# Kernel optimization log

Measured on AMD Instinct MI355X. Metric: run time of the kernel, lower is better.

Reference implementation:

```python
import jax, jax.numpy as jnp
import numpy as np

NUM_EXPERTS = 64
TOP_K = 6
EP_SIZE = 8
EP_RANK = 0
N_LOCAL = NUM_EXPERTS // EP_SIZE  # 8 local experts on this rank
HIDDEN = 2048
INTER = 1408
BLOCK_N = 128
BLOCK_K = 128
T = 2048  # tokens


def setup_inputs() -> dict:
    key = jax.random.key(0)
    ks = jax.random.split(key, 6)
    return {
        "x": jax.random.normal(ks[0], (T, HIDDEN), jnp.float32),
        "router_logits": jax.random.normal(ks[1], (T, NUM_EXPERTS), jnp.float32),
        "w13": jax.random.normal(ks[2], (N_LOCAL, 2 * INTER, HIDDEN), jnp.float32) * 0.02,
        "w13_scale": jax.random.uniform(ks[3], (N_LOCAL, 2 * INTER // BLOCK_N, HIDDEN // BLOCK_K), jnp.float32, 0.5, 1.5),
        "w2": jax.random.normal(ks[4], (N_LOCAL, HIDDEN, INTER), jnp.float32) * 0.02,
        "w2_scale": jax.random.uniform(ks[5], (N_LOCAL, HIDDEN // BLOCK_N, INTER // BLOCK_K), jnp.float32, 0.5, 1.5),
    }


def _dequant(w, s, bn, bk):
    # block-quantized weight dequant: w[e, n, k] * s[e, n//bn, k//bk]
    s_full = jnp.repeat(jnp.repeat(s, bn, axis=1), bk, axis=2)
    return w * s_full


def reference(x, router_logits, w13, w13_scale, w2, w2_scale):
    # --- top-k routing (softmax -> topk -> renormalize) ---
    probs = jax.nn.softmax(router_logits, axis=-1)           # [T, E]
    topk_w, topk_ids = jax.lax.top_k(probs, TOP_K)           # [T, K]
    topk_w = topk_w / jnp.sum(topk_w, axis=-1, keepdims=True)
    # --- expert-id remap to local partition (balanced map: e % ep_size) ---
    eids = jnp.arange(NUM_EXPERTS)
    expert_id_to_local = jnp.where(eids % EP_SIZE == EP_RANK, eids // EP_SIZE, -1)
    local_ids = expert_id_to_local[topk_ids]                 # [T, K], -1 if off-rank
    valid = local_ids >= 0
    # combine weights per local expert: comb[t, e] = sum_k topk_w[t,k] * [local==e]
    tok = jnp.arange(x.shape[0])[:, None]
    comb = jnp.zeros((x.shape[0], N_LOCAL), x.dtype).at[
        tok, jnp.where(valid, local_ids, 0)
    ].add(jnp.where(valid, topk_w, 0.0))
    # --- dequantize block-quantized weights ---
    w13_dq = _dequant(w13, w13_scale, BLOCK_N, BLOCK_K)      # [E, 2I, H]
    w2_dq = _dequant(w2, w2_scale, BLOCK_N, BLOCK_K)         # [E, H, I]
    # --- grouped GEMM (dense over local experts, masked by comb) ---
    h = jnp.einsum('th,enh->etn', x, w13_dq)                 # [E, T, 2I]
    gate, up = h[..., :INTER], h[..., INTER:]
    a = jax.nn.silu(gate) * up                               # [E, T, I]
    o = jnp.einsum('etn,ehn->eth', a, w2_dq)                 # [E, T, H]
    return jnp.einsum('eth,te->th', o, comb)                 # [T, H]
```

## Files before the change

### kernel.cpp

```cpp
#include <hip/hip_runtime.h>
#include <hip/hip_bf16.h>
#include <cstdint>

#define T_TOK 2048
#define HID   2048
#define NEXP  64
#define TOPK  6
#define NLOC  8
#define ITR   1408
#define ITR2  2816
#define NSLOT (T_TOK * TOPK)
#define NK1   32
#define NK2   22

#define OFF_CNT   0
#define OFF_CNT2  32
#define OFF_OFFS  64
#define OFF_TOPID 4096
#define OFF_TOPW  (OFF_TOPID + T_TOK * TOPK * 4)
#define OFF_TOK   (OFF_TOPW  + T_TOK * TOPK * 4)
#define OFF_WOF   (OFF_TOK   + NSLOT * 4)
#define OFF_XBF   (OFF_WOF   + NSLOT * 4)
#define OFF_ABUF  (OFF_XBF   + (size_t)T_TOK * HID * 2)

typedef __attribute__((ext_vector_type(4))) float f32x4;
typedef __attribute__((ext_vector_type(8))) short s16x8;
typedef __attribute__((ext_vector_type(4))) short s16x4;

__device__ __forceinline__ short f2bf(float f) {
    union { float f; unsigned u; } v; v.f = f;
    unsigned r = v.u + 0x7FFFu + ((v.u >> 16) & 1u);
    return (short)(r >> 16);
}

__global__ __launch_bounds__(256) void k_zero(float* __restrict__ out,
                                              int* __restrict__ cnt)
{
    const int idx = blockIdx.x * 256 + threadIdx.x;
    float4 z = {0.f, 0.f, 0.f, 0.f};
    #pragma unroll
    for (int p = 0; p < 4; ++p)
        *(float4*)&out[(size_t)(idx + p * 262144) * 4] = z;
    if (blockIdx.x == 0 && threadIdx.x < 16) cnt[threadIdx.x] = 0;
}

__global__ __launch_bounds__(256) void k_route(
    const float* __restrict__ logits, int* __restrict__ cnt,
    int* __restrict__ top_ids, float* __restrict__ top_w)
{
    const int lane = threadIdx.x & 63;
    const int t = blockIdx.x * 4 + (threadIdx.x >> 6);

    float v = logits[t * NEXP + lane];
    float m = v;
    #pragma unroll
    for (int s = 32; s > 0; s >>= 1) m = fmaxf(m, __shfl_xor(m, s));
    float ev = expf(v - m);
    float ssum = ev;
    #pragma unroll
    for (int s = 32; s > 0; s >>= 1) ssum += __shfl_xor(ssum, s);
    float p = ev / ssum;

    float pv = p;
    int ids[TOPK]; float wsel[TOPK]; float wsum = 0.f;
    #pragma unroll
    for (int i = 0; i < TOPK; ++i) {
        float mx = pv;
        #pragma unroll
        for (int s = 32; s > 0; s >>= 1) mx = fmaxf(mx, __shfl_xor(mx, s));
        unsigned long long b = __ballot(pv == mx);
        int idx = (int)__builtin_ctzll(b);
        float w = __shfl(p, idx);
        ids[i] = idx; wsel[i] = w; wsum += w;
        if (lane == idx) pv = -1.0f;
    }
    if (lane < TOPK) {
        top_ids[t * TOPK + lane] = ids[lane];
        top_w[t * TOPK + lane]  = wsel[lane] / wsum;
    }
    if (lane == 0) {
        #pragma unroll
        for (int i = 0; i < TOPK; ++i)
            if ((ids[i] & 7) == 0) atomicAdd(&cnt[ids[i] >> 3], 1);
    }
}

__global__ void k_offsets(int* __restrict__ cnt, int* __restrict__ cnt2,
                          int* __restrict__ offs)
{
    if (threadIdx.x == 0) {
        int s = 0;
        for (int e = 0; e < NLOC; ++e) { offs[e] = s; s += cnt[e]; cnt2[e] = 0; }
    }
}

__global__ __launch_bounds__(256) void k_scatter(
    const int* __restrict__ top_ids, const float* __restrict__ top_w,
    const int* __restrict__ offs, int* __restrict__ cnt2,
    int* __restrict__ tok_of, float* __restrict__ w_of)
{
    const int t = blockIdx.x * 256 + threadIdx.x;
    #pragma unroll
    for (int i = 0; i < TOPK; ++i) {
        int id = top_ids[t * TOPK + i];
        if ((id & 7) == 0) {
            int e = id >> 3;
            int s = offs[e] + atomicAdd(&cnt2[e], 1);
            tok_of[s] = t;
            w_of[s]  = top_w[t * TOPK + i];
        }
    }
}

__global__ __launch_bounds__(256) void k_cvt_x(const float* __restrict__ x,
                                               short* __restrict__ xbf)
{
    const int r = blockIdx.x;
    const int c = threadIdx.x * 8;
    const float4 a = *(const float4*)&x[(size_t)r * HID + c];
    const float4 b = *(const float4*)&x[(size_t)r * HID + c + 4];
    s16x8 v = { f2bf(a.x), f2bf(a.y), f2bf(a.z), f2bf(a.w),
                f2bf(b.x), f2bf(b.y), f2bf(b.z), f2bf(b.w) };
    *(s16x8*)&xbf[(size_t)r * HID + c] = v;
}

__global__ __launch_bounds__(256, 2) void k_gemm1(
    const short* __restrict__ xbf, const float* __restrict__ w13,
    const float* __restrict__ w13s, const int* __restrict__ offs,
    const int* __restrict__ cnt, const int* __restrict__ tok_of,
    short* __restrict__ a_buf)
{
    const int b = blockIdx.x;
    const int e = b & 7;
    const int tt = b >> 3;
    const int cntE = cnt[e];
    const int m0 = (tt / 44) * 256;
    if (m0 >= cntE) return;
    const int n0p = (tt % 44) * 32;
    const int base = offs[e] + m0;
    const int tid = threadIdx.x;
    const int lane = tid & 63;
    const int wm = tid >> 6;

    __shared__ __align__(16) short As[2][256 * 64];
    __shared__ __align__(16) short Ws[2][64 * 64];

    int* tokp = (int*)&As[0][0];
    tokp[tid] = tok_of[base + ((m0 + tid < cntE) ? tid : 0)];
    __syncthreads();

    const short* aptr[8];
    int aoff[8];
    #pragma unroll
    for (int p = 0; p < 8; ++p) {
        const int row = p * 32 + (tid >> 3), cg = tid & 7;
        aptr[p] = xbf + (size_t)tokp[row] * HID + cg * 8;
        aoff[p] = (row * 64 + cg * 8) ^ ((row & 7) << 3);
    }
    __syncthreads();

    const float* wptr[4];
    int woff[4];
    {
        const float* wg = w13 + ((size_t)e * ITR2 + n0p) * HID;
        const float* wu = w13 + ((size_t)e * ITR2 + ITR + n0p) * HID;
        #pragma unroll
        for (int p = 0; p < 4; ++p) {
            const int row = p * 16 + (tid >> 4), ch = tid & 15;
            wptr[p] = ((p < 2) ? wg : wu) + (size_t)(row & 31) * HID + ch * 4;
            woff[p] = (row * 64 + ch * 4) ^ ((row & 7) << 3);
        }
    }
    const int sgi = (e * 22 + (n0p >> 7)) * 16;
    const int sui = (e * 22 + 11 + (n0p >> 7)) * 16;

    s16x8 ra[8];
    float4 rw[4];
    float sgv, suv;
    f32x4 acc[2][2][4] = {};

#define G1_LOAD(kk) do {                                                       \
    const int k0 = (kk) * 64;                                                  \
    sgv = w13s[sgi + ((kk) >> 1)];                                             \
    suv = w13s[sui + ((kk) >> 1)];                                             \
    _Pragma("unroll")                                                          \
    for (int p = 0; p < 8; ++p) ra[p] = *(const s16x8*)(aptr[p] + k0);         \
    _Pragma("unroll")                                                          \
    for (int p = 0; p < 4; ++p) rw[p] = *(const float4*)(wptr[p] + k0);        \
} while (0)

#define G1_WRITE(b) do {                                                       \
    _Pragma("unroll")                                                          \
    for (int p = 0; p < 8; ++p) *(s16x8*)&As[b][aoff[p]] = ra[p];              \
    _Pragma("unroll")                                                          \
    for (int p = 0; p < 4; ++p) {                                              \
        const float s = (p < 2) ? sgv : suv;                                   \
        s16x4 v = { f2bf(rw[p].x * s), f2bf(rw[p].y * s),                      \
                    f2bf(rw[p].z * s), f2bf(rw[p].w * s) };                    \
        *(s16x4*)&Ws[b][woff[p]] = v;                                          \
    }                                                                          \
} while (0)

#define G1_COMP(b) do {                                                        \
    _Pragma("unroll")                                                          \
    for (int ks = 0; ks < 2; ++ks) {                                           \
        const int co = ks * 32 + (lane >> 4) * 8;                              \
        s16x8 af[4];                                                           \
        _Pragma("unroll")                                                      \
        for (int mf = 0; mf < 4; ++mf) {                                       \
            const int row = wm * 64 + mf * 16 + (lane & 15);                   \
            af[mf] = *(const s16x8*)&As[b][(row * 64 + co) ^ ((row & 7) << 3)];\
        }                                                                      \
        _Pragma("unroll")                                                      \
        for (int t = 0; t < 2; ++t)                                            \
        _Pragma("unroll")                                                      \
        for (int nf = 0; nf < 2; ++nf) {                                       \
            const int row = t * 32 + nf * 16 + (lane & 15);                    \
            s16x8 bv = *(const s16x8*)&Ws[b][(row * 64 + co) ^ ((row & 7) << 3)];\
            _Pragma("unroll")                                                  \
            for (int mf = 0; mf < 4; ++mf)                                     \
                acc[t][nf][mf] = __builtin_amdgcn_mfma_f32_16x16x32_bf16(af[mf], bv, acc[t][nf][mf], 0, 0, 0); \
        }                                                                      \
    }                                                                          \
} while (0)

    G1_LOAD(0);
    G1_WRITE(0);
    __syncthreads();
    #pragma unroll 2
    for (int k = 0; k < NK1; ++k) {
        if (k + 1 < NK1) G1_LOAD(k + 1);
        G1_COMP(k & 1);
        if (k + 1 < NK1) {
            G1_WRITE((k & 1) ^ 1);
            __syncthreads();
        }
    }

    #pragma unroll
    for (int nf = 0; nf < 2; ++nf) {
        const int col = n0p + nf * 16 + (lane & 15);
        #pragma unroll
        for (int mf = 0; mf < 4; ++mf)
        #pragma unroll
        for (int j = 0; j < 4; ++j) {
            const int row = wm * 64 + mf * 16 + (lane >> 4) * 4 + j;
            if (m0 + row < cntE) {
                const float g = acc[0][nf][mf][j], u = acc[1][nf][mf][j];
                const float a = (g / (1.f + __expf(-g))) * u;
                a_buf[(size_t)(base + row) * ITR + col] = f2bf(a);
            }
        }
    }
#undef G1_LOAD
#undef G1_WRITE
#undef G1_COMP
}

__global__ __launch_bounds__(256, 2) void k_gemm2(
    const short* __restrict__ a_buf, const float* __restrict__ w2,
    const float* __restrict__ w2s, const int* __restrict__ offs,
    const int* __restrict__ cnt, const int* __restrict__ tok_of,
    const float* __restrict__ w_of, float* __restrict__ out)
{
    const int b = blockIdx.x;
    const int e = b & 7;
    const int tt = b >> 3;
    const int cntE = cnt[e];
    const int m0 = (tt / 64) * 256;
    if (m0 >= cntE) return;
    const int n0 = (tt % 64) * 32;
    const int base = offs[e] + m0;
    const int tid = threadIdx.x;
    const int lane = tid & 63;
    const int wm = tid >> 6;

    __shared__ __align__(16) short As[2][256 * 64];
    __shared__ __align__(16) short Ws[2][32 * 64];

    const short* aptr[8];
    int aoff[8];
    #pragma unroll
    for (int p = 0; p < 8; ++p) {
        const int row = p * 32 + (tid >> 3), cg = tid & 7;
        int srow = base + row; if (srow > NSLOT - 1) srow = NSLOT - 1;
        aptr[p] = a_buf + (size_t)srow * ITR + cg * 8;
        aoff[p] = (row * 64 + cg * 8) ^ ((row & 7) << 3);
    }
    const float* wptr[2];
    int woff[2];
    #pragma unroll
    for (int p = 0; p < 2; ++p) {
        const int row = p * 16 + (tid >> 4), ch = tid & 15;
        wptr[p] = w2 + ((size_t)e * HID + n0 + row) * ITR + ch * 4;
        woff[p] = (row * 64 + ch * 4) ^ ((row & 7) << 3);
    }
    const int sci = (e * 16 + (n0 >> 7)) * 11;

    s16x8 ra[8];
    float4 rw[2];
    float scv;
    f32x4 acc[2][4] = {};

#define G2_LOAD(kk) do {                                                       \
    const int k0 = (kk) * 64;                                                  \
    scv = w2s[sci + ((kk) >> 1)];                                              \
    _Pragma("unroll")                                                          \
    for (int p = 0; p < 8; ++p) ra[p] = *(const s16x8*)(aptr[p] + k0);         \
    _Pragma("unroll")                                                          \
    for (int p = 0; p < 2; ++p) rw[p] = *(const float4*)(wptr[p] + k0);        \
} while (0)

#define G2_WRITE(b) do {                                                       \
    _Pragma("unroll")                                                          \
    for (int p = 0; p < 8; ++p) *(s16x8*)&As[b][aoff[p]] = ra[p];              \
    _Pragma("unroll")                                                          \
    for (int p = 0; p < 2; ++p) {                                              \
        s16x4 v = { f2bf(rw[p].x * scv), f2bf(rw[p].y * scv),                  \
                    f2bf(rw[p].z * scv), f2bf(rw[p].w * scv) };                \
        *(s16x4*)&Ws[b][woff[p]] = v;                                          \
    }                                                                          \
} while (0)

#define G2_COMP(b) do {                                                        \
    _Pragma("unroll")                                                          \
    for (int ks = 0; ks < 2; ++ks) {                                           \
        const int co = ks * 32 + (lane >> 4) * 8;                              \
        s16x8 af[4];                                                           \
        _Pragma("unroll")                                                      \
        for (int mf = 0; mf < 4; ++mf) {                                       \
            const int row = wm * 64 + mf * 16 + (lane & 15);                   \
            af[mf] = *(const s16x8*)&As[b][(row * 64 + co) ^ ((row & 7) << 3)];\
        }                                                                      \
        _Pragma("unroll")                                                      \
        for (int nf = 0; nf < 2; ++nf) {                                       \
            const int row = nf * 16 + (lane & 15);                             \
            s16x8 bv = *(const s16x8*)&Ws[b][(row * 64 + co) ^ ((row & 7) << 3)];\
            _Pragma("unroll")                                                  \
            for (int mf = 0; mf < 4; ++mf)                                     \
                acc[nf][mf] = __builtin_amdgcn_mfma_f32_16x16x32_bf16(af[mf], bv, acc[nf][mf], 0, 0, 0); \
        }                                                                      \
    }                                                                          \
} while (0)

    G2_LOAD(0);
    G2_WRITE(0);
    __syncthreads();
    #pragma unroll 2
    for (int k = 0; k < NK2; ++k) {
        if (k + 1 < NK2) G2_LOAD(k + 1);
        G2_COMP(k & 1);
        if (k + 1 < NK2) {
            G2_WRITE((k & 1) ^ 1);
            __syncthreads();
        }
    }

    #pragma unroll
    for (int mf = 0; mf < 4; ++mf)
    #pragma unroll
    for (int j = 0; j < 4; ++j) {
        const int row = wm * 64 + mf * 16 + (lane >> 4) * 4 + j;
        if (m0 + row < cntE) {
            const int   t = tok_of[base + row];
            const float w = w_of[base + row];
            #pragma unroll
            for (int nf = 0; nf < 2; ++nf) {
                const int col = n0 + nf * 16 + (lane & 15);
                atomicAdd(&out[(size_t)t * HID + col], acc[nf][mf][j] * w);
            }
        }
    }
#undef G2_LOAD
#undef G2_WRITE
#undef G2_COMP
}

extern "C" void kernel_launch(void* const* d_in, const int* in_sizes, int n_in,
                              void* d_out, int out_size, void* d_ws, size_t ws_size,
                              hipStream_t stream)
{
    const float* x      = (const float*)d_in[0];
    const float* logits = (const float*)d_in[1];
    const float* w13    = (const float*)d_in[2];
    const float* w13s   = (const float*)d_in[3];
    const float* w2     = (const float*)d_in[4];
    const float* w2s    = (const float*)d_in[5];
    float* out = (float*)d_out;
    char*  ws  = (char*)d_ws;

    int*   cnt     = (int*)(ws + OFF_CNT);
    int*   cnt2    = (int*)(ws + OFF_CNT2);
    int*   offs    = (int*)(ws + OFF_OFFS);
    int*   top_ids = (int*)(ws + OFF_TOPID);
    float* top_w   = (float*)(ws + OFF_TOPW);
    int*   tok_of  = (int*)(ws + OFF_TOK);
    float* w_of    = (float*)(ws + OFF_WOF);
    short* xbf     = (short*)(ws + OFF_XBF);
    short* a_buf   = (short*)(ws + OFF_ABUF);

    k_zero   <<<1024,        256, 0, stream>>>(out, cnt);
    k_route  <<<T_TOK / 4,   256, 0, stream>>>(logits, cnt, top_ids, top_w);
    k_offsets<<<1,            64, 0, stream>>>(cnt, cnt2, offs);
    k_scatter<<<T_TOK / 256, 256, 0, stream>>>(top_ids, top_w, offs, cnt2, tok_of, w_of);
    k_cvt_x  <<<T_TOK,       256, 0, stream>>>(x, xbf);
    k_gemm1  <<<44 * 8 * NLOC, 256, 0, stream>>>(xbf, w13, w13s, offs, cnt, tok_of, a_buf);
    k_gemm2  <<<64 * 8 * NLOC, 256, 0, stream>>>(a_buf, w2, w2s, offs, cnt, tok_of, w_of, out);
}
```

Baseline: 168.3 us.

## Fuse prep kernels, inline expert offsets, and pipeline GEMM loads across LDS-only barriers

Folds x-to-bf16 conversion and output zeroing into one prep kernel. Drops the single-thread offsets kernel: each scatter and GEMM block now recomputes its expert offset from the counts, which removes two kernel launches. Both GEMMs get explicit two-set register double buffering and a custom barrier that waits only on LDS counters. Outstanding global loads for the next tile can then stay in flight across the barrier, where __syncthreads would wait for them. This raises register pressure under the 2-blocks-per-CU launch bound and depends on the compiler inserting correct vmcnt waits before the register values are used.

After: 192.3 us. 1.14x slower.

```diff
diff --git a/kernel.cpp b/kernel.cpp
--- a/kernel.cpp
+++ b/kernel.cpp
@@ -33,15 +33,28 @@
     return (short)(r >> 16);
 }
 
-__global__ __launch_bounds__(256) void k_zero(float* __restrict__ out,
+#define BAR() do {                                            \
+    asm volatile("s_waitcnt lgkmcnt(0)" ::: "memory");        \
+    __builtin_amdgcn_s_barrier();                             \
+    asm volatile("" ::: "memory");                            \
+} while (0)
+
+__global__ __launch_bounds__(256) void k_prep(const float* __restrict__ x,
+                                              short* __restrict__ xbf,
+                                              float* __restrict__ out,
                                               int* __restrict__ cnt)
 {
-    const int idx = blockIdx.x * 256 + threadIdx.x;
+    const int r = blockIdx.x;
+    const int c = threadIdx.x * 8;
+    const float4 a = *(const float4*)&x[(size_t)r * HID + c];
+    const float4 b = *(const float4*)&x[(size_t)r * HID + c + 4];
+    s16x8 v = { f2bf(a.x), f2bf(a.y), f2bf(a.z), f2bf(a.w),
+                f2bf(b.x), f2bf(b.y), f2bf(b.z), f2bf(b.w) };
+    *(s16x8*)&xbf[(size_t)r * HID + c] = v;
     float4 z = {0.f, 0.f, 0.f, 0.f};
-    #pragma unroll
-    for (int p = 0; p < 4; ++p)
-        *(float4*)&out[(size_t)(idx + p * 262144) * 4] = z;
-    if (blockIdx.x == 0 && threadIdx.x < 16) cnt[threadIdx.x] = 0;
+    *(float4*)&out[(size_t)r * HID + c] = z;
+    *(float4*)&out[(size_t)r * HID + c + 4] = z;
+    if (r == 0 && threadIdx.x < 16) cnt[threadIdx.x] = 0;
 }
 
 __global__ __launch_bounds__(256) void k_route(
@@ -85,21 +98,18 @@
     }
 }
 
-__global__ void k_offsets(int* __restrict__ cnt, int* __restrict__ cnt2,
-                          int* __restrict__ offs)
-{
-    if (threadIdx.x == 0) {
-        int s = 0;
-        for (int e = 0; e < NLOC; ++e) { offs[e] = s; s += cnt[e]; cnt2[e] = 0; }
-    }
-}
-
 __global__ __launch_bounds__(256) void k_scatter(
     const int* __restrict__ top_ids, const float* __restrict__ top_w,
-    const int* __restrict__ offs, int* __restrict__ cnt2,
+    const int* __restrict__ cnt, int* __restrict__ cnt2,
     int* __restrict__ tok_of, float* __restrict__ w_of)
 {
     const int t = blockIdx.x * 256 + threadIdx.x;
+    int offs[NLOC];
+    {
+        int s = 0;
+        #pragma unroll
+        for (int i = 0; i < NLOC; ++i) { offs[i] = s; s += cnt[i]; }
+    }
     #pragma unroll
     for (int i = 0; i < TOPK; ++i) {
         int id = top_ids[t * TOPK + i];
@@ -112,32 +122,21 @@
     }
 }
 
-__global__ __launch_bounds__(256) void k_cvt_x(const float* __restrict__ x,
-                                               short* __restrict__ xbf)
-{
-    const int r = blockIdx.x;
-    const int c = threadIdx.x * 8;
-    const float4 a = *(const float4*)&x[(size_t)r * HID + c];
-    const float4 b = *(const float4*)&x[(size_t)r * HID + c + 4];
-    s16x8 v = { f2bf(a.x), f2bf(a.y), f2bf(a.z), f2bf(a.w),
-                f2bf(b.x), f2bf(b.y), f2bf(b.z), f2bf(b.w) };
-    *(s16x8*)&xbf[(size_t)r * HID + c] = v;
-}
-
 __global__ __launch_bounds__(256, 2) void k_gemm1(
     const short* __restrict__ xbf, const float* __restrict__ w13,
-    const float* __restrict__ w13s, const int* __restrict__ offs,
-    const int* __restrict__ cnt, const int* __restrict__ tok_of,
-    short* __restrict__ a_buf)
+    const float* __restrict__ w13s, const int* __restrict__ cnt,
+    const int* __restrict__ tok_of, short* __restrict__ a_buf)
 {
     const int b = blockIdx.x;
     const int e = b & 7;
     const int tt = b >> 3;
-    const int cntE = cnt[e];
+    int off_e = 0, cntE = 0;
+    #pragma unroll
+    for (int i = 0; i < NLOC; ++i) { int c = cnt[i]; if (i < e) off_e += c; if (i == e) cntE = c; }
     const int m0 = (tt / 44) * 256;
     if (m0 >= cntE) return;
     const int n0p = (tt % 44) * 32;
-    const int base = offs[e] + m0;
+    const int base = off_e + m0;
     const int tid = threadIdx.x;
     const int lane = tid & 63;
     const int wm = tid >> 6;
@@ -147,7 +146,7 @@
 
     int* tokp = (int*)&As[0][0];
     tokp[tid] = tok_of[base + ((m0 + tid < cntE) ? tid : 0)];
-    __syncthreads();
+    BAR();
 
     const short* aptr[8];
     int aoff[8];
@@ -157,7 +156,7 @@
         aptr[p] = xbf + (size_t)tokp[row] * HID + cg * 8;
         aoff[p] = (row * 64 + cg * 8) ^ ((row & 7) << 3);
     }
-    __syncthreads();
+    BAR();
 
     const float* wptr[4];
     int woff[4];
@@ -174,29 +173,29 @@
     const int sgi = (e * 22 + (n0p >> 7)) * 16;
     const int sui = (e * 22 + 11 + (n0p >> 7)) * 16;
 
-    s16x8 ra[8];
-    float4 rw[4];
-    float sgv, suv;
+    s16x8 ra0[8], ra1[8];
+    float4 rw0[4], rw1[4];
+    float sg0, su0, sg1, su1;
     f32x4 acc[2][2][4] = {};
 
-#define G1_LOAD(kk) do {                                                       \
+#define G1_LOAD(kk, S) do {                                                    \
     const int k0 = (kk) * 64;                                                  \
-    sgv = w13s[sgi + ((kk) >> 1)];                                             \
-    suv = w13s[sui + ((kk) >> 1)];                                             \
-    _Pragma("unroll")                                                          \
-    for (int p = 0; p < 8; ++p) ra[p] = *(const s16x8*)(aptr[p] + k0);         \
-    _Pragma("unroll")                                                          \
-    for (int p = 0; p < 4; ++p) rw[p] = *(const float4*)(wptr[p] + k0);        \
-} while (0)
-
-#define G1_WRITE(b) do {                                                       \
-    _Pragma("unroll")                                                          \
-    for (int p = 0; p < 8; ++p) *(s16x8*)&As[b][aoff[p]] = ra[p];              \
+    sg##S = w13s[sgi + ((kk) >> 1)];                                           \
+    su##S = w13s[sui + ((kk) >> 1)];                                           \
+    _Pragma("unroll")                                                          \
+    for (int p = 0; p < 8; ++p) ra##S[p] = *(const s16x8*)(aptr[p] + k0);      \
+    _Pragma("unroll")                                                          \
+    for (int p = 0; p < 4; ++p) rw##S[p] = *(const float4*)(wptr[p] + k0);     \
+} while (0)
+
+#define G1_WRITE(b, S) do {                                                    \
+    _Pragma("unroll")                                                          \
+    for (int p = 0; p < 8; ++p) *(s16x8*)&As[b][aoff[p]] = ra##S[p];           \
     _Pragma("unroll")                                                          \
     for (int p = 0; p < 4; ++p) {                                              \
-        const float s = (p < 2) ? sgv : suv;                                   \
-        s16x4 v = { f2bf(rw[p].x * s), f2bf(rw[p].y * s),                      \
-                    f2bf(rw[p].z * s), f2bf(rw[p].w * s) };                    \
+        const float s = (p < 2) ? sg##S : su##S;                               \
+        s16x4 v = { f2bf(rw##S[p].x * s), f2bf(rw##S[p].y * s),                \
+                    f2bf(rw##S[p].z * s), f2bf(rw##S[p].w * s) };              \
         *(s16x4*)&Ws[b][woff[p]] = v;                                          \
     }                                                                          \
 } while (0)
@@ -224,18 +223,24 @@
     }                                                                          \
 } while (0)
 
-    G1_LOAD(0);
-    G1_WRITE(0);
-    __syncthreads();
-    #pragma unroll 2
-    for (int k = 0; k < NK1; ++k) {
-        if (k + 1 < NK1) G1_LOAD(k + 1);
-        G1_COMP(k & 1);
-        if (k + 1 < NK1) {
-            G1_WRITE((k & 1) ^ 1);
-            __syncthreads();
-        }
-    }
+    G1_LOAD(0, 0);
+    G1_WRITE(0, 0);
+    G1_LOAD(1, 1);
+    BAR();
+    for (int k = 0; k < NK1 - 2; k += 2) {
+        G1_LOAD(k + 2, 0);
+        G1_COMP(0);
+        G1_WRITE(1, 1);
+        BAR();
+        G1_LOAD(k + 3, 1);
+        G1_COMP(1);
+        G1_WRITE(0, 0);
+        BAR();
+    }
+    G1_COMP(0);
+    G1_WRITE(1, 1);
+    BAR();
+    G1_COMP(1);
 
     #pragma unroll
     for (int nf = 0; nf < 2; ++nf) {
@@ -259,18 +264,20 @@
 
 __global__ __launch_bounds__(256, 2) void k_gemm2(
     const short* __restrict__ a_buf, const float* __restrict__ w2,
-    const float* __restrict__ w2s, const int* __restrict__ offs,
-    const int* __restrict__ cnt, const int* __restrict__ tok_of,
-    const float* __restrict__ w_of, float* __restrict__ out)
+    const float* __restrict__ w2s, const int* __restrict__ cnt,
+    const int* __restrict__ tok_of, const float* __restrict__ w_of,
+    float* __restrict__ out)
 {
     const int b = blockIdx.x;
     const int e = b & 7;
     const int tt = b >> 3;
-    const int cntE = cnt[e];
+    int off_e = 0, cntE = 0;
+    #pragma unroll
+    for (int i = 0; i < NLOC; ++i) { int c = cnt[i]; if (i < e) off_e += c; if (i == e) cntE = c; }
     const int m0 = (tt / 64) * 256;
     if (m0 >= cntE) return;
     const int n0 = (tt % 64) * 32;
-    const int base = offs[e] + m0;
+    const int base = off_e + m0;
     const int tid = threadIdx.x;
     const int lane = tid & 63;
     const int wm = tid >> 6;
@@ -297,27 +304,27 @@
     }
     const int sci = (e * 16 + (n0 >> 7)) * 11;
 
-    s16x8 ra[8];
-    float4 rw[2];
-    float scv;
+    s16x8 ra0[8], ra1[8];
+    float4 rw0[2], rw1[2];
+    float sc0, sc1;
     f32x4 acc[2][4] = {};
 
-#define G2_LOAD(kk) do {                                                       \
+#define G2_LOAD(kk, S) do {                                                    \
     const int k0 = (kk) * 64;                                                  \
-    scv = w2s[sci + ((kk) >> 1)];                                              \
-    _Pragma("unroll")                                                          \
-    for (int p = 0; p < 8; ++p) ra[p] = *(const s16x8*)(aptr[p] + k0);         \
-    _Pragma("unroll")                                                          \
-    for (int p = 0; p < 2; ++p) rw[p] = *(const float4*)(wptr[p] + k0);        \
-} while (0)
-
-#define G2_WRITE(b) do {                                                       \
-    _Pragma("unroll")                                                          \
-    for (int p = 0; p < 8; ++p) *(s16x8*)&As[b][aoff[p]] = ra[p];              \
+    sc##S = w2s[sci + ((kk) >> 1)];                                            \
+    _Pragma("unroll")                                                          \
+    for (int p = 0; p < 8; ++p) ra##S[p] = *(const s16x8*)(aptr[p] + k0);      \
+    _Pragma("unroll")                                                          \
+    for (int p = 0; p < 2; ++p) rw##S[p] = *(const float4*)(wptr[p] + k0);     \
+} while (0)
+
+#define G2_WRITE(b, S) do {                                                    \
+    _Pragma("unroll")                                                          \
+    for (int p = 0; p < 8; ++p) *(s16x8*)&As[b][aoff[p]] = ra##S[p];           \
     _Pragma("unroll")                                                          \
     for (int p = 0; p < 2; ++p) {                                              \
-        s16x4 v = { f2bf(rw[p].x * scv), f2bf(rw[p].y * scv),                  \
-                    f2bf(rw[p].z * scv), f2bf(rw[p].w * scv) };                \
+        s16x4 v = { f2bf(rw##S[p].x * sc##S), f2bf(rw##S[p].y * sc##S),        \
+                    f2bf(rw##S[p].z * sc##S), f2bf(rw##S[p].w * sc##S) };      \
         *(s16x4*)&Ws[b][woff[p]] = v;                                          \
     }                                                                          \
 } while (0)
@@ -343,18 +350,24 @@
     }                                                                          \
 } while (0)
 
-    G2_LOAD(0);
-    G2_WRITE(0);
-    __syncthreads();
-    #pragma unroll 2
-    for (int k = 0; k < NK2; ++k) {
-        if (k + 1 < NK2) G2_LOAD(k + 1);
-        G2_COMP(k & 1);
-        if (k + 1 < NK2) {
-            G2_WRITE((k & 1) ^ 1);
-            __syncthreads();
-        }
-    }
+    G2_LOAD(0, 0);
+    G2_WRITE(0, 0);
+    G2_LOAD(1, 1);
+    BAR();
+    for (int k = 0; k < NK2 - 2; k += 2) {
+        G2_LOAD(k + 2, 0);
+        G2_COMP(0);
+        G2_WRITE(1, 1);
+        BAR();
+        G2_LOAD(k + 3, 1);
+        G2_COMP(1);
+        G2_WRITE(0, 0);
+        BAR();
+    }
+    G2_COMP(0);
+    G2_WRITE(1, 1);
+    BAR();
+    G2_COMP(1);
 
     #pragma unroll
     for (int mf = 0; mf < 4; ++mf)
@@ -391,7 +404,6 @@
 
     int*   cnt     = (int*)(ws + OFF_CNT);
     int*   cnt2    = (int*)(ws + OFF_CNT2);
-    int*   offs    = (int*)(ws + OFF_OFFS);
     int*   top_ids = (int*)(ws + OFF_TOPID);
     float* top_w   = (float*)(ws + OFF_TOPW);
     int*   tok_of  = (int*)(ws + OFF_TOK);
@@ -399,11 +411,9 @@
     short* xbf     = (short*)(ws + OFF_XBF);
     short* a_buf   = (short*)(ws + OFF_ABUF);
 
-    k_zero   <<<1024,        256, 0, stream>>>(out, cnt);
+    k_prep   <<<T_TOK,       256, 0, stream>>>(x, xbf, out, cnt);
     k_route  <<<T_TOK / 4,   256, 0, stream>>>(logits, cnt, top_ids, top_w);
-    k_offsets<<<1,            64, 0, stream>>>(cnt, cnt2, offs);
-    k_scatter<<<T_TOK / 256, 256, 0, stream>>>(top_ids, top_w, offs, cnt2, tok_of, w_of);
-    k_cvt_x  <<<T_TOK,       256, 0, stream>>>(x, xbf);
-    k_gemm1  <<<44 * 8 * NLOC, 256, 0, stream>>>(xbf, w13, w13s, offs, cnt, tok_of, a_buf);
-    k_gemm2  <<<64 * 8 * NLOC, 256, 0, stream>>>(a_buf, w2, w2s, offs, cnt, tok_of, w_of, out);
-}
+    k_scatter<<<T_TOK / 256, 256, 0, stream>>>(top_ids, top_w, cnt, cnt2, tok_of, w_of);
+    k_gemm1  <<<44 * 8 * NLOC, 256, 0, stream>>>(xbf, w13, w13s, cnt, tok_of, a_buf);
+    k_gemm2  <<<64 * 8 * NLOC, 256, 0, stream>>>(a_buf, w2, w2s, cnt, tok_of, w_of, out);
+}
```

## Halve GEMM M-tile, fuse zero/convert kernels, inline expert offsets

Applied to the files above, without the earlier changes.

Both grouped-GEMM kernels drop from 256-row to 128-row token tiles. This doubles the block grid and raises the occupancy hint (3 and 4 blocks per CU) to improve parallelism and reduce padding waste for roughly 190 tokens per expert. The output-zeroing and x-to-bf16 conversion kernels are merged into one, and the separate offsets kernel is removed: each consumer now computes its expert's prefix sum from the counts. The cost is that each weight tile may be streamed twice per expert, which adds fp32 weight traffic unless the second read hits in cache.

New measurement: 141.6 us. -15.9%, faster.

```diff
diff --git a/kernel.cpp b/kernel.cpp
--- a/kernel.cpp
+++ b/kernel.cpp
@@ -15,7 +15,6 @@
 
 #define OFF_CNT   0
 #define OFF_CNT2  32
-#define OFF_OFFS  64
 #define OFF_TOPID 4096
 #define OFF_TOPW  (OFF_TOPID + T_TOK * TOPK * 4)
 #define OFF_TOK   (OFF_TOPW  + T_TOK * TOPK * 4)
@@ -33,15 +32,22 @@
     return (short)(r >> 16);
 }
 
-__global__ __launch_bounds__(256) void k_zero(float* __restrict__ out,
+__global__ __launch_bounds__(256) void k_prep(const float* __restrict__ x,
+                                              short* __restrict__ xbf,
+                                              float* __restrict__ out,
                                               int* __restrict__ cnt)
 {
-    const int idx = blockIdx.x * 256 + threadIdx.x;
+    const int r = blockIdx.x;
+    const int c = threadIdx.x * 8;
+    const float4 a = *(const float4*)&x[(size_t)r * HID + c];
+    const float4 b = *(const float4*)&x[(size_t)r * HID + c + 4];
+    s16x8 v = { f2bf(a.x), f2bf(a.y), f2bf(a.z), f2bf(a.w),
+                f2bf(b.x), f2bf(b.y), f2bf(b.z), f2bf(b.w) };
+    *(s16x8*)&xbf[(size_t)r * HID + c] = v;
     float4 z = {0.f, 0.f, 0.f, 0.f};
-    #pragma unroll
-    for (int p = 0; p < 4; ++p)
-        *(float4*)&out[(size_t)(idx + p * 262144) * 4] = z;
-    if (blockIdx.x == 0 && threadIdx.x < 16) cnt[threadIdx.x] = 0;
+    *(float4*)&out[(size_t)r * HID + c] = z;
+    *(float4*)&out[(size_t)r * HID + c + 4] = z;
+    if (r == 0 && threadIdx.x < 16) cnt[threadIdx.x] = 0;
 }
 
 __global__ __launch_bounds__(256) void k_route(
@@ -85,21 +91,18 @@
     }
 }
 
-__global__ void k_offsets(int* __restrict__ cnt, int* __restrict__ cnt2,
-                          int* __restrict__ offs)
-{
-    if (threadIdx.x == 0) {
-        int s = 0;
-        for (int e = 0; e < NLOC; ++e) { offs[e] = s; s += cnt[e]; cnt2[e] = 0; }
-    }
-}
-
 __global__ __launch_bounds__(256) void k_scatter(
     const int* __restrict__ top_ids, const float* __restrict__ top_w,
-    const int* __restrict__ offs, int* __restrict__ cnt2,
+    const int* __restrict__ cnt, int* __restrict__ cnt2,
     int* __restrict__ tok_of, float* __restrict__ w_of)
 {
     const int t = blockIdx.x * 256 + threadIdx.x;
+    int offs[NLOC];
+    {
+        int s = 0;
+        #pragma unroll
+        for (int i = 0; i < NLOC; ++i) { offs[i] = s; s += cnt[i]; }
+    }
     #pragma unroll
     for (int i = 0; i < TOPK; ++i) {
         int id = top_ids[t * TOPK + i];
@@ -112,47 +115,36 @@
     }
 }
 
-__global__ __launch_bounds__(256) void k_cvt_x(const float* __restrict__ x,
-                                               short* __restrict__ xbf)
-{
-    const int r = blockIdx.x;
-    const int c = threadIdx.x * 8;
-    const float4 a = *(const float4*)&x[(size_t)r * HID + c];
-    const float4 b = *(const float4*)&x[(size_t)r * HID + c + 4];
-    s16x8 v = { f2bf(a.x), f2bf(a.y), f2bf(a.z), f2bf(a.w),
-                f2bf(b.x), f2bf(b.y), f2bf(b.z), f2bf(b.w) };
-    *(s16x8*)&xbf[(size_t)r * HID + c] = v;
-}
-
-__global__ __launch_bounds__(256, 2) void k_gemm1(
+__global__ __launch_bounds__(256, 3) void k_gemm1(
     const short* __restrict__ xbf, const float* __restrict__ w13,
-    const float* __restrict__ w13s, const int* __restrict__ offs,
-    const int* __restrict__ cnt, const int* __restrict__ tok_of,
-    short* __restrict__ a_buf)
+    const float* __restrict__ w13s, const int* __restrict__ cnt,
+    const int* __restrict__ tok_of, short* __restrict__ a_buf)
 {
     const int b = blockIdx.x;
     const int e = b & 7;
     const int tt = b >> 3;
-    const int cntE = cnt[e];
-    const int m0 = (tt / 44) * 256;
+    int off_e = 0, cntE = 0;
+    #pragma unroll
+    for (int i = 0; i < NLOC; ++i) { int c = cnt[i]; if (i < e) off_e += c; if (i == e) cntE = c; }
+    const int m0 = (tt / 44) * 128;
     if (m0 >= cntE) return;
     const int n0p = (tt % 44) * 32;
-    const int base = offs[e] + m0;
+    const int base = off_e + m0;
     const int tid = threadIdx.x;
     const int lane = tid & 63;
     const int wm = tid >> 6;
 
-    __shared__ __align__(16) short As[2][256 * 64];
+    __shared__ __align__(16) short As[2][128 * 64];
     __shared__ __align__(16) short Ws[2][64 * 64];
 
     int* tokp = (int*)&As[0][0];
-    tokp[tid] = tok_of[base + ((m0 + tid < cntE) ? tid : 0)];
+    if (tid < 128) tokp[tid] = tok_of[base + ((m0 + tid < cntE) ? tid : 0)];
     __syncthreads();
 
-    const short* aptr[8];
-    int aoff[8];
-    #pragma unroll
-    for (int p = 0; p < 8; ++p) {
+    const short* aptr[4];
+    int aoff[4];
+    #pragma unroll
+    for (int p = 0; p < 4; ++p) {
         const int row = p * 32 + (tid >> 3), cg = tid & 7;
         aptr[p] = xbf + (size_t)tokp[row] * HID + cg * 8;
         aoff[p] = (row * 64 + cg * 8) ^ ((row & 7) << 3);
@@ -174,24 +166,24 @@
     const int sgi = (e * 22 + (n0p >> 7)) * 16;
     const int sui = (e * 22 + 11 + (n0p >> 7)) * 16;
 
-    s16x8 ra[8];
+    s16x8 ra[4];
     float4 rw[4];
     float sgv, suv;
-    f32x4 acc[2][2][4] = {};
+    f32x4 acc[2][2][2] = {};
 
 #define G1_LOAD(kk) do {                                                       \
     const int k0 = (kk) * 64;                                                  \
     sgv = w13s[sgi + ((kk) >> 1)];                                             \
     suv = w13s[sui + ((kk) >> 1)];                                             \
     _Pragma("unroll")                                                          \
-    for (int p = 0; p < 8; ++p) ra[p] = *(const s16x8*)(aptr[p] + k0);         \
+    for (int p = 0; p < 4; ++p) ra[p] = *(const s16x8*)(aptr[p] + k0);         \
     _Pragma("unroll")                                                          \
     for (int p = 0; p < 4; ++p) rw[p] = *(const float4*)(wptr[p] + k0);        \
 } while (0)
 
 #define G1_WRITE(b) do {                                                       \
     _Pragma("unroll")                                                          \
-    for (int p = 0; p < 8; ++p) *(s16x8*)&As[b][aoff[p]] = ra[p];              \
+    for (int p = 0; p < 4; ++p) *(s16x8*)&As[b][aoff[p]] = ra[p];              \
     _Pragma("unroll")                                                          \
     for (int p = 0; p < 4; ++p) {                                              \
         const float s = (p < 2) ? sgv : suv;                                   \
@@ -205,10 +197,10 @@
     _Pragma("unroll")                                                          \
     for (int ks = 0; ks < 2; ++ks) {                                           \
         const int co = ks * 32 + (lane >> 4) * 8;                              \
-        s16x8 af[4];                                                           \
+        s16x8 af[2];                                                           \
         _Pragma("unroll")                                                      \
-        for (int mf = 0; mf < 4; ++mf) {                                       \
-            const int row = wm * 64 + mf * 16 + (lane & 15);                   \
+        for (int mf = 0; mf < 2; ++mf) {                                       \
+            const int row = wm * 32 + mf * 16 + (lane & 15);                   \
             af[mf] = *(const s16x8*)&As[b][(row * 64 + co) ^ ((row & 7) << 3)];\
         }                                                                      \
         _Pragma("unroll")                                                      \
@@ -218,7 +210,7 @@
             const int row = t * 32 + nf * 16 + (lane & 15);                    \
             s16x8 bv = *(const s16x8*)&Ws[b][(row * 64 + co) ^ ((row & 7) << 3)];\
             _Pragma("unroll")                                                  \
-            for (int mf = 0; mf < 4; ++mf)                                     \
+            for (int mf = 0; mf < 2; ++mf)                                     \
                 acc[t][nf][mf] = __builtin_amdgcn_mfma_f32_16x16x32_bf16(af[mf], bv, acc[t][nf][mf], 0, 0, 0); \
         }                                                                      \
     }                                                                          \
@@ -241,10 +233,10 @@
     for (int nf = 0; nf < 2; ++nf) {
         const int col = n0p + nf * 16 + (lane & 15);
         #pragma unroll
-        for (int mf = 0; mf < 4; ++mf)
+        for (int mf = 0; mf < 2; ++mf)
         #pragma unroll
         for (int j = 0; j < 4; ++j) {
-            const int row = wm * 64 + mf * 16 + (lane >> 4) * 4 + j;
+            const int row = wm * 32 + mf * 16 + (lane >> 4) * 4 + j;
             if (m0 + row < cntE) {
                 const float g = acc[0][nf][mf][j], u = acc[1][nf][mf][j];
                 const float a = (g / (1.f + __expf(-g))) * u;
@@ -257,31 +249,33 @@
 #undef G1_COMP
 }
 
-__global__ __launch_bounds__(256, 2) void k_gemm2(
+__global__ __launch_bounds__(256, 4) void k_gemm2(
     const short* __restrict__ a_buf, const float* __restrict__ w2,
-    const float* __restrict__ w2s, const int* __restrict__ offs,
-    const int* __restrict__ cnt, const int* __restrict__ tok_of,
-    const float* __restrict__ w_of, float* __restrict__ out)
+    const float* __restrict__ w2s, const int* __restrict__ cnt,
+    const int* __restrict__ tok_of, const float* __restrict__ w_of,
+    float* __restrict__ out)
 {
     const int b = blockIdx.x;
     const int e = b & 7;
     const int tt = b >> 3;
-    const int cntE = cnt[e];
-    const int m0 = (tt / 64) * 256;
+    int off_e = 0, cntE = 0;
+    #pragma unroll
+    for (int i = 0; i < NLOC; ++i) { int c = cnt[i]; if (i < e) off_e += c; if (i == e) cntE = c; }
+    const int m0 = (tt / 64) * 128;
     if (m0 >= cntE) return;
     const int n0 = (tt % 64) * 32;
-    const int base = offs[e] + m0;
+    const int base = off_e + m0;
     const int tid = threadIdx.x;
     const int lane = tid & 63;
     const int wm = tid >> 6;
 
-    __shared__ __align__(16) short As[2][256 * 64];
+    __shared__ __align__(16) short As[2][128 * 64];
     __shared__ __align__(16) short Ws[2][32 * 64];
 
-    const short* aptr[8];
-    int aoff[8];
-    #pragma unroll
-    for (int p = 0; p < 8; ++p) {
+    const short* aptr[4];
+    int aoff[4];
+    #pragma unroll
+    for (int p = 0; p < 4; ++p) {
         const int row = p * 32 + (tid >> 3), cg = tid & 7;
         int srow = base + row; if (srow > NSLOT - 1) srow = NSLOT - 1;
         aptr[p] = a_buf + (size_t)srow * ITR + cg * 8;
@@ -297,23 +291,23 @@
     }
     const int sci = (e * 16 + (n0 >> 7)) * 11;
 
-    s16x8 ra[8];
+    s16x8 ra[4];
     float4 rw[2];
     float scv;
-    f32x4 acc[2][4] = {};
+    f32x4 acc[2][2] = {};
 
 #define G2_LOAD(kk) do {                                                       \
     const int k0 = (kk) * 64;                                                  \
     scv = w2s[sci + ((kk) >> 1)];                                              \
     _Pragma("unroll")                                                          \
-    for (int p = 0; p < 8; ++p) ra[p] = *(const s16x8*)(aptr[p] + k0);         \
+    for (int p = 0; p < 4; ++p) ra[p] = *(const s16x8*)(aptr[p] + k0);         \
     _Pragma("unroll")                                                          \
     for (int p = 0; p < 2; ++p) rw[p] = *(const float4*)(wptr[p] + k0);        \
 } while (0)
 
 #define G2_WRITE(b) do {                                                       \
     _Pragma("unroll")                                                          \
-    for (int p = 0; p < 8; ++p) *(s16x8*)&As[b][aoff[p]] = ra[p];              \
+    for (int p = 0; p < 4; ++p) *(s16x8*)&As[b][aoff[p]] = ra[p];              \
     _Pragma("unroll")                                                          \
     for (int p = 0; p < 2; ++p) {                                              \
         s16x4 v = { f2bf(rw[p].x * scv), f2bf(rw[p].y * scv),                  \
@@ -326,10 +320,10 @@
     _Pragma("unroll")                                                          \
     for (int ks = 0; ks < 2; ++ks) {                                           \
         const int co = ks * 32 + (lane >> 4) * 8;                              \
-        s16x8 af[4];                                                           \
+        s16x8 af[2];                                                           \
         _Pragma("unroll")                                                      \
-        for (int mf = 0; mf < 4; ++mf) {                                       \
-            const int row = wm * 64 + mf * 16 + (lane & 15);                   \
+        for (int mf = 0; mf < 2; ++mf) {                                       \
+            const int row = wm * 32 + mf * 16 + (lane & 15);                   \
             af[mf] = *(const s16x8*)&As[b][(row * 64 + co) ^ ((row & 7) << 3)];\
         }                                                                      \
         _Pragma("unroll")                                                      \
@@ -337,7 +331,7 @@
             const int row = nf * 16 + (lane & 15);                             \
             s16x8 bv = *(const s16x8*)&Ws[b][(row * 64 + co) ^ ((row & 7) << 3)];\
             _Pragma("unroll")                                                  \
-            for (int mf = 0; mf < 4; ++mf)                                     \
+            for (int mf = 0; mf < 2; ++mf)                                     \
                 acc[nf][mf] = __builtin_amdgcn_mfma_f32_16x16x32_bf16(af[mf], bv, acc[nf][mf], 0, 0, 0); \
         }                                                                      \
     }                                                                          \
@@ -357,10 +351,10 @@
     }
 
     #pragma unroll
-    for (int mf = 0; mf < 4; ++mf)
+    for (int mf = 0; mf < 2; ++mf)
     #pragma unroll
     for (int j = 0; j < 4; ++j) {
-        const int row = wm * 64 + mf * 16 + (lane >> 4) * 4 + j;
+        const int row = wm * 32 + mf * 16 + (lane >> 4) * 4 + j;
         if (m0 + row < cntE) {
             const int   t = tok_of[base + row];
             const float w = w_of[base + row];
@@ -391,7 +385,6 @@
 
     int*   cnt     = (int*)(ws + OFF_CNT);
     int*   cnt2    = (int*)(ws + OFF_CNT2);
-    int*   offs    = (int*)(ws + OFF_OFFS);
     int*   top_ids = (int*)(ws + OFF_TOPID);
     float* top_w   = (float*)(ws + OFF_TOPW);
     int*   tok_of  = (int*)(ws + OFF_TOK);
@@ -399,11 +392,9 @@
     short* xbf     = (short*)(ws + OFF_XBF);
     short* a_buf   = (short*)(ws + OFF_ABUF);
 
-    k_zero   <<<1024,        256, 0, stream>>>(out, cnt);
+    k_prep   <<<T_TOK,       256, 0, stream>>>(x, xbf, out, cnt);
     k_route  <<<T_TOK / 4,   256, 0, stream>>>(logits, cnt, top_ids, top_w);
-    k_offsets<<<1,            64, 0, stream>>>(cnt, cnt2, offs);
-    k_scatter<<<T_TOK / 256, 256, 0, stream>>>(top_ids, top_w, offs, cnt2, tok_of, w_of);
-    k_cvt_x  <<<T_TOK,       256, 0, stream>>>(x, xbf);
-    k_gemm1  <<<44 * 8 * NLOC, 256, 0, stream>>>(xbf, w13, w13s, offs, cnt, tok_of, a_buf);
-    k_gemm2  <<<64 * 8 * NLOC, 256, 0, stream>>>(a_buf, w2, w2s, offs, cnt, tok_of, w_of, out);
-}
+    k_scatter<<<T_TOK / 256, 256, 0, stream>>>(top_ids, top_w, cnt, cnt2, tok_of, w_of);
+    k_gemm1  <<<44 * 16 * 8, 256, 0, stream>>>(xbf, w13, w13s, cnt, tok_of, a_buf);
+    k_gemm2  <<<64 * 16 * 8, 256, 0, stream>>>(a_buf, w2, w2s, cnt, tok_of, w_of, out);
+}
```
